# Kernel tuning notes

Hardware: AMD Instinct MI355X
Metric: run time of the kernel (lower is better)

The kernel has to match this reference:

```python
import jax, jax.numpy as jnp
import numpy as np
import math

NUM_HEADS = 16
GRID_SIZE = 32
NUM_BUCKETS = 32
MAX_DISTANCE = 128
EMBED_DIM = 1024


def _rel_pos_bucket(rel, num_buckets, max_distance):
    # T5-style bucketing, as written in the source (int truncation of log branch)
    is_neg = (rel < 0).astype(jnp.int32)
    rel = jnp.abs(rel)
    rel = jnp.clip(rel, 0, max_distance - 1)
    max_exact = num_buckets // 2
    log_branch = max_exact + (
        jnp.log(rel.astype(jnp.float32) / max_exact)
        / math.log(max_distance / max_exact)
        * (num_buckets - max_exact)
    ).astype(jnp.int32)
    bucket = is_neg * num_buckets + jnp.where(rel < max_exact, rel.astype(jnp.int32), log_branch)
    return bucket  # in [0, 2*num_buckets)


def setup_inputs() -> dict:
    key = jax.random.key(0)
    ks = jax.random.split(key, 9)
    B, N, D = 4, GRID_SIZE * GRID_SIZE, EMBED_DIM
    s = 0.02
    return {
        "query": jax.random.normal(ks[0], (B, N, D), jnp.float32),
        "key": jax.random.normal(ks[1], (B, N, D), jnp.float32),
        "value": jax.random.normal(ks[2], (B, N, D), jnp.float32),
        "in_proj_w": jax.random.normal(ks[3], (3 * D, D), jnp.float32) * s,
        "in_proj_b": jnp.zeros((3 * D,), jnp.float32),
        "out_proj_w": jax.random.normal(ks[4], (D, D), jnp.float32) * s,
        "out_proj_b": jnp.zeros((D,), jnp.float32),
        "rel_bias_table": jax.random.normal(ks[5], (2 * NUM_BUCKETS, NUM_HEADS), jnp.float32) * s,
    }


def reference(query, key, value, in_proj_w, in_proj_b, out_proj_w, out_proj_b, rel_bias_table):
    B, N, D = query.shape
    H = NUM_HEADS
    hd = D // H
    scaling = hd ** -0.5

    # in_proj applied to `query` only (source ignores key/value args)
    qkv = query @ in_proj_w.T + in_proj_b          # [B, N, 3D]
    q, k, v = jnp.split(qkv, 3, axis=-1)
    q = q.reshape(B, N, H, hd).transpose(0, 2, 1, 3)  # [B, H, N, hd]
    k = k.reshape(B, N, H, hd).transpose(0, 2, 1, 3)
    v = v.reshape(B, N, H, hd).transpose(0, 2, 1, 3)

    attn = jnp.einsum("bhnd,bhmd->bhnm", q, k) * scaling  # [B, H, N, N]

    # 2D relative-position bucket bias
    idx = jnp.arange(N)
    row = idx // GRID_SIZE
    col = idx % GRID_SIZE
    row_bucket = _rel_pos_bucket(row[:, None] - row[None, :], NUM_BUCKETS, MAX_DISTANCE)
    col_bucket = _rel_pos_bucket(col[:, None] - col[None, :], NUM_BUCKETS, MAX_DISTANCE)
    bias = rel_bias_table[row_bucket] + rel_bias_table[col_bucket]  # [N, N, H]
    attn = attn + bias.transpose(2, 0, 1)[None]  # [B, H, N, N]

    attn_weights = jax.nn.softmax(attn, axis=-1)
    out = jnp.einsum("bhnm,bhmd->bhnd", attn_weights, v)  # [B, H, N, hd]
    out = out.transpose(0, 2, 1, 3).reshape(B, N, D)
    out = out @ out_proj_w.T + out_proj_b
    return out, attn_weights
```

## Files before the change

### kernel.cpp

```cpp
#include <hip/hip_runtime.h>
#include <hip/hip_bf16.h>

typedef __attribute__((ext_vector_type(8))) short bf16x8;
typedef __attribute__((ext_vector_type(4))) float f32x4;
typedef __attribute__((ext_vector_type(4))) unsigned short us4;

#define MFMA16(a,b,c) __builtin_amdgcn_mfma_f32_16x16x32_bf16((a),(b),(c),0,0,0)

__device__ __forceinline__ unsigned short f2bf(float f){
  unsigned u = __builtin_bit_cast(unsigned, f);
  u += 0x7fffu + ((u>>16)&1u);
  return (unsigned short)(u>>16);
}
__device__ __forceinline__ float bf2f(unsigned short h){
  unsigned u = ((unsigned)h)<<16;
  return __builtin_bit_cast(float, u);
}
__device__ __forceinline__ void gload_lds16(const unsigned short* g, unsigned short* l){
  __builtin_amdgcn_global_load_lds((const __attribute__((address_space(1))) void*)g,
                                   (__attribute__((address_space(3))) void*)l,
                                   16, 0, 0);
}

__global__ __launch_bounds__(256) void cast_all(
    const float* __restrict__ q, const float* __restrict__ wi, const float* __restrict__ wo,
    unsigned short* __restrict__ qq, unsigned short* __restrict__ wib, unsigned short* __restrict__ wob)
{
  int i4 = (blockIdx.x*256 + threadIdx.x)*4;
  const float* src; unsigned short* dst; int off;
  if (i4 < 4194304)       { src=q;  dst=qq;  off=i4; }
  else if (i4 < 7340032)  { src=wi; dst=wib; off=i4-4194304; }
  else                    { src=wo; dst=wob; off=i4-7340032; }
  float4 v = *(const float4*)(src+off);
  us4 o; o.x=f2bf(v.x); o.y=f2bf(v.y); o.z=f2bf(v.z); o.w=f2bf(v.w);
  *(us4*)(dst+off) = o;
}

__global__ __launch_bounds__(256) void gemm_qkv(
    const unsigned short* __restrict__ A, const unsigned short* __restrict__ Bw,
    const float* __restrict__ bias,
    unsigned short* __restrict__ qo, unsigned short* __restrict__ ko, unsigned short* __restrict__ vTo)
{
  __shared__ unsigned short lA[128*64];
  __shared__ unsigned short lB[128*64];
  int tid = threadIdx.x, lane = tid&63, w = tid>>6;
  int wr = (w>>1)<<6, wc = (w&1)<<6;
  int rowT = blockIdx.y<<7, colT = blockIdx.x<<7;
  f32x4 acc[4][4] = {};
  for (int k0=0; k0<1024; k0+=64){
    #pragma unroll
    for (int it=0; it<4; ++it){
      int ci = it*256+tid; int r=ci>>3, cs=ci&7;
      int c = (cs ^ (r&7))<<3;
      gload_lds16(A + (size_t)(rowT+r)*1024 + k0 + c, &lA[ci<<3]);
    }
    #pragma unroll
    for (int it=0; it<4; ++it){
      int ci = it*256+tid; int r=ci>>3, cs=ci&7;
      int c = (cs ^ (r&7))<<3;
      gload_lds16(Bw + (size_t)(colT+r)*1024 + k0 + c, &lB[ci<<3]);
    }
    asm volatile("s_waitcnt vmcnt(0)" ::: "memory");
    __syncthreads();
    #pragma unroll
    for (int kk=0; kk<2; ++kk){
      int kc = (kk<<2) + (lane>>4);
      bf16x8 a[4], b[4];
      #pragma unroll
      for (int i=0;i<4;++i){
        int r = wr + (i<<4) + (lane&15);
        a[i] = *(const bf16x8*)&lA[(r<<6) + ((kc ^ (r&7))<<3)];
      }
      #pragma unroll
      for (int j=0;j<4;++j){
        int r = wc + (j<<4) + (lane&15);
        b[j] = *(const bf16x8*)&lB[(r<<6) + ((kc ^ (r&7))<<3)];
      }
      #pragma unroll
      for (int i=0;i<4;++i)
        #pragma unroll
        for (int j=0;j<4;++j)
          acc[i][j] = MFMA16(a[i], b[j], acc[i][j]);
    }
    __syncthreads();
  }
  int sec = colT >> 10;
  #pragma unroll
  for (int i=0;i<4;++i){
    #pragma unroll
    for (int j=0;j<4;++j){
      int cg = colT + wc + (j<<4) + (lane&15);
      int d = cg & 1023, hh = d>>6, di = d&63;
      float bsv = bias[cg];
      #pragma unroll
      for (int q=0;q<4;++q){
        int m = rowT + wr + (i<<4) + ((lane>>4)<<2) + q;
        int b = m>>10, n = m&1023;
        unsigned short bv = f2bf(acc[i][j][q] + bsv);
        size_t bh = (size_t)((b<<4) + hh);
        if (sec==0)      qo[(bh<<16) + ((size_t)n<<6) + di] = bv;
        else if (sec==1) ko[(bh<<16) + ((size_t)n<<6) + di] = bv;
        else             vTo[(bh<<16) + ((size_t)di<<10) + n] = bv;
      }
    }
  }
}

__global__ __launch_bounds__(256) void gemm_out(
    const unsigned short* __restrict__ A, const unsigned short* __restrict__ Bw,
    const float* __restrict__ bias, float* __restrict__ out)
{
  __shared__ unsigned short lA[128*64];
  __shared__ unsigned short lB[128*64];
  int tid = threadIdx.x, lane = tid&63, w = tid>>6;
  int wr = (w>>1)<<6, wc = (w&1)<<6;
  int rowT = blockIdx.y<<7, colT = blockIdx.x<<7;
  f32x4 acc[4][4] = {};
  for (int k0=0; k0<1024; k0+=64){
    #pragma unroll
    for (int it=0; it<4; ++it){
      int ci = it*256+tid; int r=ci>>3, cs=ci&7;
      int c = (cs ^ (r&7))<<3;
      gload_lds16(A + (size_t)(rowT+r)*1024 + k0 + c, &lA[ci<<3]);
    }
    #pragma unroll
    for (int it=0; it<4; ++it){
      int ci = it*256+tid; int r=ci>>3, cs=ci&7;
      int c = (cs ^ (r&7))<<3;
      gload_lds16(Bw + (size_t)(colT+r)*1024 + k0 + c, &lB[ci<<3]);
    }
    asm volatile("s_waitcnt vmcnt(0)" ::: "memory");
    __syncthreads();
    #pragma unroll
    for (int kk=0; kk<2; ++kk){
      int kc = (kk<<2) + (lane>>4);
      bf16x8 a[4], b[4];
      #pragma unroll
      for (int i=0;i<4;++i){
        int r = wr + (i<<4) + (lane&15);
        a[i] = *(const bf16x8*)&lA[(r<<6) + ((kc ^ (r&7))<<3)];
      }
      #pragma unroll
      for (int j=0;j<4;++j){
        int r = wc + (j<<4) + (lane&15);
        b[j] = *(const bf16x8*)&lB[(r<<6) + ((kc ^ (r&7))<<3)];
      }
      #pragma unroll
      for (int i=0;i<4;++i)
        #pragma unroll
        for (int j=0;j<4;++j)
          acc[i][j] = MFMA16(a[i], b[j], acc[i][j]);
    }
    __syncthreads();
  }
  #pragma unroll
  for (int i=0;i<4;++i){
    #pragma unroll
    for (int j=0;j<4;++j){
      int cg = colT + wc + (j<<4) + (lane&15);
      float bsv = bias[cg];
      #pragma unroll
      for (int q=0;q<4;++q){
        int m = rowT + wr + (i<<4) + ((lane>>4)<<2) + q;
        out[(size_t)m*1024 + cg] = acc[i][j][q] + bsv;
      }
    }
  }
}

__global__ __launch_bounds__(256) void attn_fused(
    const unsigned short* __restrict__ qbf, const unsigned short* __restrict__ kbf,
    const unsigned short* __restrict__ vT, const float* __restrict__ tbl,
    float* __restrict__ attn_out, unsigned short* __restrict__ oa)
{
  __shared__ unsigned short P[64*1024];
  __shared__ unsigned short qs[64*64];
  __shared__ float biasv[64];
  __shared__ float rsum[4][64];
  __shared__ float rinv_s[64];

  int tid=threadIdx.x, lane=tid&63, w=tid>>6;
  int pair = blockIdx.x >> 4;
  int stripe = blockIdx.x & 15;
  int h = pair & 15;
  int bg = pair >> 4;
  int nbase = stripe<<6;
  const unsigned short* qg = qbf + ((size_t)pair<<16) + ((size_t)nbase<<6);
  const unsigned short* kg = kbf + ((size_t)pair<<16);
  const unsigned short* vg = vT  + ((size_t)pair<<16);

  if (tid < 63){
    int dd = tid - 31;
    int neg = dd<0 ? 1:0;
    int a = dd<0 ? -dd : dd;
    if (a>127) a=127;
    int bkt;
    if (a<16) bkt = a;
    else bkt = 16 + (int)(__logf((float)a*(1.f/16.f)) * (16.f/__logf(8.f)));
    bkt += neg*32;
    biasv[tid] = tbl[(bkt<<4) + h];
  }
  #pragma unroll
  for (int it=0; it<2; ++it){
    int ci = it*256+tid; int r=ci>>3, cs=ci&7;
    int c = (cs ^ (r&7))<<3;
    gload_lds16(qg + (r<<6) + c, &qs[ci<<3]);
  }
  asm volatile("s_waitcnt vmcnt(0)" ::: "memory");
  __syncthreads();

  float rs[16];
  #pragma unroll
  for (int z=0;z<16;++z) rs[z]=0.f;
  int colW = w<<8;
  for (int ct=0; ct<16; ++ct){
    int cb = colW + (ct<<4);
    const unsigned short* kp = kg + ((size_t)(cb + (lane&15))<<6) + ((lane>>4)<<3);
    bf16x8 bk0 = *(const bf16x8*)kp;
    bf16x8 bk1 = *(const bf16x8*)(kp+32);
    f32x4 acc[4] = {};
    #pragma unroll
    for (int rt=0; rt<4; ++rt){
      int r = (rt<<4) + (lane&15);
      int base = r<<6;
      bf16x8 a0 = *(const bf16x8*)&qs[base + (((lane>>4)      ^ (r&7))<<3)];
      bf16x8 a1 = *(const bf16x8*)&qs[base + (((4+(lane>>4))  ^ (r&7))<<3)];
      acc[rt] = MFMA16(a0, bk0, acc[rt]);
      acc[rt] = MFMA16(a1, bk1, acc[rt]);
    }
    int j = cb + (lane&15);
    int jr = j>>5, jc = j&31;
    #pragma unroll
    for (int rt=0; rt<4; ++rt){
      #pragma unroll
      for (int q=0;q<4;++q){
        int r = (rt<<4) + ((lane>>4)<<2) + q;
        int i = nbase + r;
        float lg = acc[rt][q]*0.125f + biasv[(i>>5)-jr+31] + biasv[(i&31)-jc+31];
        float e = __expf(lg);
        rs[rt*4+q] += e;
        int byteoff = (r<<11) + ((((j>>3) ^ (r&7)))<<4) + ((j&7)<<1);
        *(unsigned short*)((char*)P + byteoff) = f2bf(e);
      }
    }
  }
  #pragma unroll
  for (int z=0; z<16; ++z){
    float v = rs[z];
    v += __shfl_xor(v,1); v += __shfl_xor(v,2); v += __shfl_xor(v,4); v += __shfl_xor(v,8);
    rs[z] = v;
  }
  if ((lane&15)==0){
    #pragma unroll
    for (int rt=0;rt<4;++rt)
      #pragma unroll
      for (int q=0;q<4;++q)
        rsum[w][(rt<<4)+((lane>>4)<<2)+q] = rs[rt*4+q];
  }
  __syncthreads();
  if (tid<64) rinv_s[tid] = 1.f/(rsum[0][tid]+rsum[1][tid]+rsum[2][tid]+rsum[3][tid]);
  __syncthreads();

  float* ao = attn_out + ((size_t)pair<<20) + ((size_t)nbase<<10);
  for (int it=0; it<32; ++it){
    int r = (it<<1) + (tid>>7);
    int c8 = (tid&127)<<3;
    int byteoff = (r<<11) + ((((c8>>3) ^ (r&7)))<<4);
    bf16x8 pv8 = *(const bf16x8*)((char*)P + byteoff);
    float ri = rinv_s[r];
    float4 o0, o1;
    o0.x = bf2f((unsigned short)pv8[0])*ri;
    o0.y = bf2f((unsigned short)pv8[1])*ri;
    o0.z = bf2f((unsigned short)pv8[2])*ri;
    o0.w = bf2f((unsigned short)pv8[3])*ri;
    o1.x = bf2f((unsigned short)pv8[4])*ri;
    o1.y = bf2f((unsigned short)pv8[5])*ri;
    o1.z = bf2f((unsigned short)pv8[6])*ri;
    o1.w = bf2f((unsigned short)pv8[7])*ri;
    *(float4*)(ao + ((size_t)r<<10) + c8)     = o0;
    *(float4*)(ao + ((size_t)r<<10) + c8 + 4) = o1;
  }

  f32x4 oacc[4] = {};
  int dbase = w<<4;
  const unsigned short* vp = vg + ((size_t)(dbase + (lane&15))<<10) + ((lane>>4)<<3);
  for (int kc=0; kc<1024; kc+=32){
    bf16x8 bv = *(const bf16x8*)(vp + kc);
    int ck = (kc>>3) + (lane>>4);
    #pragma unroll
    for (int rt=0;rt<4;++rt){
      int r = (rt<<4) + (lane&15);
      bf16x8 a = *(const bf16x8*)((char*)P + (r<<11) + ((ck ^ (r&7))<<4));
      oacc[rt] = MFMA16(a, bv, oacc[rt]);
    }
  }
  #pragma unroll
  for (int rt=0;rt<4;++rt){
    #pragma unroll
    for (int q=0;q<4;++q){
      int r = (rt<<4) + ((lane>>4)<<2) + q;
      int d = dbase + (lane&15);
      float val = oacc[rt][q]*rinv_s[r];
      oa[((size_t)((bg<<10) + nbase + r)<<10) + (h<<6) + d] = f2bf(val);
    }
  }
}

extern "C" void kernel_launch(void* const* d_in, const int* in_sizes, int n_in,
                              void* d_out, int out_size, void* d_ws, size_t ws_size,
                              hipStream_t stream)
{
  const float* query = (const float*)d_in[0];
  const float* wi  = (const float*)d_in[3];
  const float* bi  = (const float*)d_in[4];
  const float* wo  = (const float*)d_in[5];
  const float* bo  = (const float*)d_in[6];
  const float* tbl = (const float*)d_in[7];

  char* ws = (char*)d_ws;
  unsigned short* qq  = (unsigned short*)(ws);
  unsigned short* wib = (unsigned short*)(ws + 8388608);
  unsigned short* wob = (unsigned short*)(ws + 14680064);
  unsigned short* qbf = (unsigned short*)(ws + 16777216);
  unsigned short* kbf = (unsigned short*)(ws + 25165824);
  unsigned short* vTb = (unsigned short*)(ws + 33554432);
  unsigned short* oa  = (unsigned short*)(ws + 41943040);

  float* out  = (float*)d_out;
  float* attn = out + 4194304;

  cast_all<<<dim3(8192), dim3(256), 0, stream>>>(query, wi, wo, qq, wib, wob);
  gemm_qkv<<<dim3(24,32), dim3(256), 0, stream>>>(qq, wib, bi, qbf, kbf, vTb);
  attn_fused<<<dim3(1024), dim3(256), 0, stream>>>(qbf, kbf, vTb, tbl, attn, oa);
  gemm_out<<<dim3(8,32), dim3(256), 0, stream>>>(oa, wob, bo, out);
}
```

Measured before the change: 205.4 us.

## Halve attention row stripe to 32 rows, remap blocks, precompute bias terms

```diff
diff --git a/kernel.cpp b/kernel.cpp
--- a/kernel.cpp
+++ b/kernel.cpp
@@ -173,18 +173,20 @@
     const unsigned short* __restrict__ vT, const float* __restrict__ tbl,
     float* __restrict__ attn_out, unsigned short* __restrict__ oa)
 {
-  __shared__ unsigned short P[64*1024];
-  __shared__ unsigned short qs[64*64];
+  __shared__ unsigned short P[32*1024];
+  __shared__ unsigned short qs[32*64];
   __shared__ float biasv[64];
-  __shared__ float rsum[4][64];
-  __shared__ float rinv_s[64];
+  __shared__ float rsum[4][32];
+  __shared__ float rinv_s[32];
 
   int tid=threadIdx.x, lane=tid&63, w=tid>>6;
-  int pair = blockIdx.x >> 4;
-  int stripe = blockIdx.x & 15;
+  int bid = blockIdx.x;
+  int wgid = ((bid&7)<<8) + (bid>>3);
+  int pair = wgid >> 5;
+  int stripe = wgid & 31;
   int h = pair & 15;
   int bg = pair >> 4;
-  int nbase = stripe<<6;
+  int nbase = stripe<<5;
   const unsigned short* qg = qbf + ((size_t)pair<<16) + ((size_t)nbase<<6);
   const unsigned short* kg = kbf + ((size_t)pair<<16);
   const unsigned short* vg = vT  + ((size_t)pair<<16);
@@ -193,76 +195,79 @@
     int dd = tid - 31;
     int neg = dd<0 ? 1:0;
     int a = dd<0 ? -dd : dd;
-    if (a>127) a=127;
     int bkt;
     if (a<16) bkt = a;
     else bkt = 16 + (int)(__logf((float)a*(1.f/16.f)) * (16.f/__logf(8.f)));
     bkt += neg*32;
     biasv[tid] = tbl[(bkt<<4) + h];
   }
-  #pragma unroll
-  for (int it=0; it<2; ++it){
-    int ci = it*256+tid; int r=ci>>3, cs=ci&7;
+  { int r=tid>>3, cs=tid&7;
     int c = (cs ^ (r&7))<<3;
-    gload_lds16(qg + (r<<6) + c, &qs[ci<<3]);
-  }
+    gload_lds16(qg + (r<<6) + c, &qs[tid<<3]); }
   asm volatile("s_waitcnt vmcnt(0)" ::: "memory");
   __syncthreads();
 
-  float rs[16];
-  #pragma unroll
-  for (int z=0;z<16;++z) rs[z]=0.f;
+  int x = lane&15, g = lane>>4;
+  float cterm[3][4];
+  #pragma unroll
+  for (int s=0;s<3;++s)
+    #pragma unroll
+    for (int q=0;q<4;++q)
+      cterm[s][q] = biasv[(g<<2) + q - x + 31 + ((s-1)<<4)];
+
+  bf16x8 qa[2][2];
+  #pragma unroll
+  for (int rt=0;rt<2;++rt){
+    int r = (rt<<4) + x;
+    #pragma unroll
+    for (int hh=0;hh<2;++hh)
+      qa[rt][hh] = *(const bf16x8*)&qs[(r<<6) + ((((hh<<2)+g) ^ (r&7))<<3)];
+  }
+
+  float rs[2][4] = {};
   int colW = w<<8;
-  for (int ct=0; ct<16; ++ct){
-    int cb = colW + (ct<<4);
-    const unsigned short* kp = kg + ((size_t)(cb + (lane&15))<<6) + ((lane>>4)<<3);
-    bf16x8 bk0 = *(const bf16x8*)kp;
-    bf16x8 bk1 = *(const bf16x8*)(kp+32);
-    f32x4 acc[4] = {};
-    #pragma unroll
-    for (int rt=0; rt<4; ++rt){
-      int r = (rt<<4) + (lane&15);
-      int base = r<<6;
-      bf16x8 a0 = *(const bf16x8*)&qs[base + (((lane>>4)      ^ (r&7))<<3)];
-      bf16x8 a1 = *(const bf16x8*)&qs[base + (((4+(lane>>4))  ^ (r&7))<<3)];
-      acc[rt] = MFMA16(a0, bk0, acc[rt]);
-      acc[rt] = MFMA16(a1, bk1, acc[rt]);
-    }
-    int j = cb + (lane&15);
-    int jr = j>>5, jc = j&31;
-    #pragma unroll
-    for (int rt=0; rt<4; ++rt){
-      #pragma unroll
-      for (int q=0;q<4;++q){
-        int r = (rt<<4) + ((lane>>4)<<2) + q;
-        int i = nbase + r;
-        float lg = acc[rt][q]*0.125f + biasv[(i>>5)-jr+31] + biasv[(i&31)-jc+31];
-        float e = __expf(lg);
-        rs[rt*4+q] += e;
-        int byteoff = (r<<11) + ((((j>>3) ^ (r&7)))<<4) + ((j&7)<<1);
-        *(unsigned short*)((char*)P + byteoff) = f2bf(e);
-      }
-    }
-  }
-  #pragma unroll
-  for (int z=0; z<16; ++z){
-    float v = rs[z];
-    v += __shfl_xor(v,1); v += __shfl_xor(v,2); v += __shfl_xor(v,4); v += __shfl_xor(v,8);
-    rs[z] = v;
-  }
-  if ((lane&15)==0){
-    #pragma unroll
-    for (int rt=0;rt<4;++rt)
-      #pragma unroll
-      for (int q=0;q<4;++q)
-        rsum[w][(rt<<4)+((lane>>4)<<2)+q] = rs[rt*4+q];
+  for (int ct2=0; ct2<8; ++ct2){
+    int cbb = colW + (ct2<<5);
+    float rterm = biasv[stripe - (cbb>>5) + 31];
+    #pragma unroll
+    for (int par=0; par<2; ++par){
+      int cb = cbb + (par<<4);
+      int j = cb + x;
+      const unsigned short* kp = kg + ((size_t)j<<6) + (g<<3);
+      bf16x8 bk0 = *(const bf16x8*)kp;
+      bf16x8 bk1 = *(const bf16x8*)(kp+32);
+      #pragma unroll
+      for (int rt=0; rt<2; ++rt){
+        f32x4 acc = {};
+        acc = MFMA16(qa[rt][0], bk0, acc);
+        acc = MFMA16(qa[rt][1], bk1, acc);
+        #pragma unroll
+        for (int q=0;q<4;++q){
+          int r = (rt<<4) + (g<<2) + q;
+          float lg = acc[q]*0.125f + rterm + cterm[rt+1-par][q];
+          float e = __expf(lg);
+          rs[rt][q] += e;
+          int byteoff = (r<<11) + ((((j>>3) ^ (r&7)))<<4) + ((j&7)<<1);
+          *(unsigned short*)((char*)P + byteoff) = f2bf(e);
+        }
+      }
+    }
+  }
+  #pragma unroll
+  for (int rt=0;rt<2;++rt){
+    #pragma unroll
+    for (int q=0;q<4;++q){
+      float v = rs[rt][q];
+      v += __shfl_xor(v,1); v += __shfl_xor(v,2); v += __shfl_xor(v,4); v += __shfl_xor(v,8);
+      if (x==0) rsum[w][(rt<<4)+(g<<2)+q] = v;
+    }
   }
   __syncthreads();
-  if (tid<64) rinv_s[tid] = 1.f/(rsum[0][tid]+rsum[1][tid]+rsum[2][tid]+rsum[3][tid]);
+  if (tid<32) rinv_s[tid] = 1.f/(rsum[0][tid]+rsum[1][tid]+rsum[2][tid]+rsum[3][tid]);
   __syncthreads();
 
   float* ao = attn_out + ((size_t)pair<<20) + ((size_t)nbase<<10);
-  for (int it=0; it<32; ++it){
+  for (int it=0; it<16; ++it){
     int r = (it<<1) + (tid>>7);
     int c8 = (tid&127)<<3;
     int byteoff = (r<<11) + ((((c8>>3) ^ (r&7)))<<4);
@@ -281,27 +286,27 @@
     *(float4*)(ao + ((size_t)r<<10) + c8 + 4) = o1;
   }
 
-  f32x4 oacc[4] = {};
+  f32x4 oacc[2] = {};
   int dbase = w<<4;
-  const unsigned short* vp = vg + ((size_t)(dbase + (lane&15))<<10) + ((lane>>4)<<3);
+  const unsigned short* vp = vg + ((size_t)(dbase + x)<<10) + (g<<3);
+  #pragma unroll 4
   for (int kc=0; kc<1024; kc+=32){
     bf16x8 bv = *(const bf16x8*)(vp + kc);
-    int ck = (kc>>3) + (lane>>4);
-    #pragma unroll
-    for (int rt=0;rt<4;++rt){
-      int r = (rt<<4) + (lane&15);
+    int ck = (kc>>3) + g;
+    #pragma unroll
+    for (int rt=0;rt<2;++rt){
+      int r = (rt<<4) + x;
       bf16x8 a = *(const bf16x8*)((char*)P + (r<<11) + ((ck ^ (r&7))<<4));
       oacc[rt] = MFMA16(a, bv, oacc[rt]);
     }
   }
   #pragma unroll
-  for (int rt=0;rt<4;++rt){
+  for (int rt=0;rt<2;++rt){
     #pragma unroll
     for (int q=0;q<4;++q){
-      int r = (rt<<4) + ((lane>>4)<<2) + q;
-      int d = dbase + (lane&15);
+      int r = (rt<<4) + (g<<2) + q;
       float val = oacc[rt][q]*rinv_s[r];
-      oa[((size_t)((bg<<10) + nbase + r)<<10) + (h<<6) + d] = f2bf(val);
+      oa[((size_t)((bg<<10) + nbase + r)<<10) + (h<<6) + dbase + x] = f2bf(val);
     }
   }
 }
@@ -331,6 +336,6 @@
 
   cast_all<<<dim3(8192), dim3(256), 0, stream>>>(query, wi, wo, qq, wib, wob);
   gemm_qkv<<<dim3(24,32), dim3(256), 0, stream>>>(qq, wib, bi, qbf, kbf, vTb);
-  attn_fused<<<dim3(1024), dim3(256), 0, stream>>>(qbf, kbf, vTb, tbl, attn, oa);
+  attn_fused<<<dim3(2048), dim3(256), 0, stream>>>(qbf, kbf, vTb, tbl, attn, oa);
   gemm_out<<<dim3(8,32), dim3(256), 0, stream>>>(oa, wob, bo, out);
 }
```

Result: faster. 193.0 us (-6.0%).
